# Optimization experiments

Measured on AMD Instinct MI355X. Metric: run time of the kernel, lower is better.

## Reference

```python
import jax, jax.numpy as jnp
import numpy as np

DT = 1.0          # ODENet default dt
W_SCALE = 0.05    # keep forward-Euler trajectory numerically tame


def setup_inputs() -> dict:
    key = jax.random.key(0)
    ks = jax.random.split(key, 4)
    T, B, H = 8192, 128, 128
    x = jax.random.normal(ks[0], (T, B, 1), dtype=jnp.float32)
    W1 = jax.random.normal(ks[1], (2, H), dtype=jnp.float32) * W_SCALE
    b1 = jnp.zeros((H,), dtype=jnp.float32)
    W2 = jax.random.normal(ks[2], (H, H), dtype=jnp.float32) * W_SCALE
    b2 = jnp.zeros((H,), dtype=jnp.float32)
    W3 = jax.random.normal(ks[3], (H, 1), dtype=jnp.float32) * W_SCALE
    b3 = jnp.zeros((1,), dtype=jnp.float32)
    return {"x": x, "W1": W1, "b1": b1, "W2": W2, "b2": b2, "W3": W3, "b3": b3}


def reference(x, W1, b1, W2, b2, W3, b3):
    # x: (T, B, 1). State y: (B,), init zeros (initial_value in ODENet.forward).
    # Forward Euler: y_{n+1} = y_n + dt * f(x_n, y_n), returning all T states
    # (y_0 included), i.e. output shape (T, B, 1) matching the input shape.
    x_sq = x[..., 0]                      # (T, B) == self.derivative_network.input
    B = x_sq.shape[1]
    y0 = jnp.zeros((B,), dtype=x.dtype)   # initial_value

    def deriv(xt, y):
        inp = jnp.stack([xt, y], axis=-1)          # (B, 2)
        h = jnp.tanh(inp @ W1 + b1)                # (B, H)
        h = jnp.tanh(h @ W2 + b2)                  # (B, H)
        return (h @ W3 + b3)[..., 0]               # (B,)

    def step(y, xt):
        y_next = y + DT * deriv(xt, y)
        return y_next, y_next

    # T-1 Euler steps produce states y_1..y_{T-1}
    _, ys = jax.lax.scan(step, y0, x_sq[:-1])      # (T-1, B)
    out = jnp.concatenate([y0[None], ys], axis=0)  # (T, B)
    return out[..., None]                          # (T, B, 1)
```

## Files before the change

### kernel.cpp

```cpp
#include <hip/hip_runtime.h>

#define T_STEPS 8192
#define BATCH   128
#define HID     128
#define NTHR    512

typedef float v2f __attribute__((ext_vector_type(2)));

__device__ __forceinline__ float fast_tanh(float z) {
    float e = __expf(2.0f * z);
    float r = __builtin_amdgcn_rcpf(1.0f + e);
    return fmaf(-2.0f, r, 1.0f);
}

__device__ __forceinline__ float quad_sum(float x) {
    int t1 = __builtin_amdgcn_update_dpp(0, __builtin_bit_cast(int, x),
                                         0xB1 , 0xf, 0xf, false);
    x += __builtin_bit_cast(float, t1);
    int t2 = __builtin_amdgcn_update_dpp(0, __builtin_bit_cast(int, x),
                                         0x4E , 0xf, 0xf, false);
    x += __builtin_bit_cast(float, t2);
    return x;
}

__device__ __forceinline__ float wave_sum_quaduniform(float x) {
#define DPP_ADD(ctrl) do {                                                        \
        int t_ = __builtin_amdgcn_update_dpp(0, __builtin_bit_cast(int, x),       \
                                             (ctrl), 0xf, 0xf, false);            \
        x += __builtin_bit_cast(float, t_); } while (0)
    DPP_ADD(0x114);
    DPP_ADD(0x118);
    DPP_ADD(0x142);
    DPP_ADD(0x143);
#undef DPP_ADD
    int s_ = __builtin_amdgcn_readlane(__builtin_bit_cast(int, x), 63);
    return __builtin_bit_cast(float, s_);
}

__device__ __forceinline__ float bcast_lane(float v, int l) {
    int r = __builtin_amdgcn_readlane(__builtin_bit_cast(int, v), l);
    return __builtin_bit_cast(float, r);
}

#define FORALL16(M) M(0) M(1) M(2) M(3) M(4) M(5) M(6) M(7) \
                    M(8) M(9) M(10) M(11) M(12) M(13) M(14) M(15)

__global__ __launch_bounds__(NTHR, 2) void odenet_scan(
    const float* __restrict__ x,
    const float* __restrict__ W1, const float* __restrict__ b1,
    const float* __restrict__ W2, const float* __restrict__ b2,
    const float* __restrict__ W3, const float* __restrict__ b3,
    float* __restrict__ out) {

    const int b    = blockIdx.x;
    const int tid  = threadIdx.x;
    const int w    = tid >> 6;
    const int lane = tid & 63;
    const int j    = (w << 4) | (lane >> 2);
    const int s    = lane & 3;

    __shared__ __align__(16) float h1buf[8][144];
    __shared__ __align__(16) float dyx[2][8];

    const float* col = W2 + j;
    const int kb = s << 5;
#define DECLW(i) v2f wp##i = {col[(kb + 2*(i) + 0) * HID],                        \
                              col[(kb + 2*(i) + 1) * HID]};
    FORALL16(DECLW)
#undef DECLW
#define PINW(i) asm volatile("" : "+v"(wp##i));
    FORALL16(PINW)
#undef PINW

    float w1xa = W1[lane],      w1ya = W1[HID + lane],      b1a = b1[lane];
    float w1xb = W1[lane + 64], w1yb = W1[HID + lane + 64], b1b = b1[lane + 64];
    float b2j = b2[j], w3j = W3[j], b3v = b3[0];
    asm volatile("" : "+v"(w1xa), "+v"(w1ya), "+v"(b1a),
                      "+v"(w1xb), "+v"(w1yb), "+v"(b1b),
                      "+v"(b2j), "+v"(w3j), "+v"(b3v));

    float y    = 0.0f;
    float ybuf = 0.0f;
    if (w == 0 && lane == 0) out[b] = 0.0f;

    float xbuf  = x[lane * BATCH + b];
    int   nb    = 64;
    float xnext = x[min(nb + lane, T_STEPS - 1) * BATCH + b];
    float xv = bcast_lane(xbuf, 0);
    float ax = fmaf(xv, w1xa, b1a);
    float bx = fmaf(xv, w1xb, b1b);

    const float4* h4 = (const float4*)&h1buf[w][s * 36];

    for (int t = 0; t < T_STEPS - 1; ++t) {
        const int tm = t & 63;

        float ha = fast_tanh(fmaf(y, w1ya, ax));
        float hb = fast_tanh(fmaf(y, w1yb, bx));
        h1buf[w][((lane >> 5)    ) * 36 + (lane & 31)] = ha;
        h1buf[w][((lane >> 5) + 2) * 36 + (lane & 31)] = hb;

        v2f a0 = {0.f, 0.f}, a1 = {0.f, 0.f}, a2 = {0.f, 0.f}, a3 = {0.f, 0.f};
        {
            float4 q0 = h4[0], q1 = h4[1], q2 = h4[2], q3 = h4[3];
            float4 q4 = h4[4], q5 = h4[5], q6 = h4[6], q7 = h4[7];
            v2f h0 = {q0.x, q0.y}, h1_ = {q0.z, q0.w};
            v2f h2 = {q1.x, q1.y}, h3 = {q1.z, q1.w};
            v2f h4v = {q2.x, q2.y}, h5 = {q2.z, q2.w};
            v2f h6 = {q3.x, q3.y}, h7 = {q3.z, q3.w};
            v2f h8 = {q4.x, q4.y}, h9 = {q4.z, q4.w};
            v2f hA = {q5.x, q5.y}, hB = {q5.z, q5.w};
            v2f hC = {q6.x, q6.y}, hD = {q6.z, q6.w};
            v2f hE = {q7.x, q7.y}, hF = {q7.z, q7.w};
            a0 += wp0 * h0;  a1 += wp1 * h1_; a2 += wp2 * h2;  a3 += wp3 * h3;
            a0 += wp4 * h4v; a1 += wp5 * h5;  a2 += wp6 * h6;  a3 += wp7 * h7;
            a0 += wp8 * h8;  a1 += wp9 * h9;  a2 += wp10 * hA; a3 += wp11 * hB;
            a0 += wp12 * hC; a1 += wp13 * hD; a2 += wp14 * hE; a3 += wp15 * hF;
        }
        v2f ap = (a0 + a1) + (a2 + a3);

        float z2  = quad_sum(ap.x + ap.y);
        float h2  = fast_tanh(z2 + b2j);
        float dyw = wave_sum_quaduniform(w3j * h2);

        if (lane == 0) dyx[t & 1][w] = dyw;

        const int tmn = (t + 1) & 63;
        if (tmn == 0) {
            xbuf = xnext;
            nb += 64;
            xnext = x[min(nb + lane, T_STEPS - 1) * BATCH + b];
        }
        float xvn = bcast_lane(xbuf, tmn);
        float axn = fmaf(xvn, w1xa, b1a);
        float bxn = fmaf(xvn, w1xb, b1b);

        asm volatile("s_waitcnt lgkmcnt(0)\n\ts_barrier" ::: "memory");

        const float4* dx4 = (const float4*)dyx[t & 1];
        float4 r0 = dx4[0], r1 = dx4[1];
        y += ((r0.x + r0.y) + (r0.z + r0.w))
           + ((r1.x + r1.y) + (r1.z + r1.w)) + b3v;

        ybuf = (lane == tm) ? y : ybuf;
        if (w == 0 && tm == 63)
            out[(t - 62 + lane) * BATCH + b] = ybuf;

        ax = axn; bx = bxn;
    }
    if (w == 0 && lane < 63)
        out[(T_STEPS - 63 + lane) * BATCH + b] = ybuf;
}

extern "C" void kernel_launch(void* const* d_in, const int* in_sizes, int n_in,
                              void* d_out, int out_size, void* d_ws, size_t ws_size,
                              hipStream_t stream) {
    const float* x  = (const float*)d_in[0];
    const float* W1 = (const float*)d_in[1];
    const float* b1 = (const float*)d_in[2];
    const float* W2 = (const float*)d_in[3];
    const float* b2 = (const float*)d_in[4];
    const float* W3 = (const float*)d_in[5];
    const float* b3 = (const float*)d_in[6];

    odenet_scan<<<dim3(BATCH), dim3(NTHR), 0, stream>>>(
        x, W1, b1, W2, b2, W3, b3, (float*)d_out);
}
```

Before: 4.015 ms.

## Halve block to 4 waves with 2-way K split per hidden unit

Each block now uses 256 threads (4 waves) instead of 512. Each lane holds 64 W2 weights in registers, and two lanes share one hidden unit where four did before. The cross-lane reduction shrinks from a quad sum to a pair sum, and the final wave reduction writes from lane 63 with no readlane. The per-step barrier synchronises fewer waves and sums fewer partials. In exchange, each lane's serial FMA chain doubles in length and register pressure rises.

After: 4.010 ms. About the same (-0.1%).

```diff
diff --git a/kernel.cpp b/kernel.cpp
--- a/kernel.cpp
+++ b/kernel.cpp
@@ -3,7 +3,7 @@
 #define T_STEPS 8192
 #define BATCH   128
 #define HID     128
-#define NTHR    512
+#define NTHR    256
 
 typedef float v2f __attribute__((ext_vector_type(2)));
 
@@ -13,28 +13,25 @@
     return fmaf(-2.0f, r, 1.0f);
 }
 
-__device__ __forceinline__ float quad_sum(float x) {
+__device__ __forceinline__ float pair_sum(float x) {
     int t1 = __builtin_amdgcn_update_dpp(0, __builtin_bit_cast(int, x),
-                                         0xB1 , 0xf, 0xf, false);
-    x += __builtin_bit_cast(float, t1);
-    int t2 = __builtin_amdgcn_update_dpp(0, __builtin_bit_cast(int, x),
-                                         0x4E , 0xf, 0xf, false);
-    x += __builtin_bit_cast(float, t2);
-    return x;
+                                         0xB1 ,
+                                         0xf, 0xf, false);
+    return x + __builtin_bit_cast(float, t1);
 }
 
-__device__ __forceinline__ float wave_sum_quaduniform(float x) {
+__device__ __forceinline__ float wave_sum_pairuniform_l63(float x) {
 #define DPP_ADD(ctrl) do {                                                        \
         int t_ = __builtin_amdgcn_update_dpp(0, __builtin_bit_cast(int, x),       \
                                              (ctrl), 0xf, 0xf, false);            \
         x += __builtin_bit_cast(float, t_); } while (0)
+    DPP_ADD(0x112);
     DPP_ADD(0x114);
     DPP_ADD(0x118);
     DPP_ADD(0x142);
     DPP_ADD(0x143);
 #undef DPP_ADD
-    int s_ = __builtin_amdgcn_readlane(__builtin_bit_cast(int, x), 63);
-    return __builtin_bit_cast(float, s_);
+    return x;
 }
 
 __device__ __forceinline__ float bcast_lane(float v, int l) {
@@ -42,8 +39,10 @@
     return __builtin_bit_cast(float, r);
 }
 
-#define FORALL16(M) M(0) M(1) M(2) M(3) M(4) M(5) M(6) M(7) \
-                    M(8) M(9) M(10) M(11) M(12) M(13) M(14) M(15)
+#define FORALL32(M) M(0) M(1) M(2) M(3) M(4) M(5) M(6) M(7) \
+                    M(8) M(9) M(10) M(11) M(12) M(13) M(14) M(15) \
+                    M(16) M(17) M(18) M(19) M(20) M(21) M(22) M(23) \
+                    M(24) M(25) M(26) M(27) M(28) M(29) M(30) M(31)
 
 __global__ __launch_bounds__(NTHR, 2) void odenet_scan(
     const float* __restrict__ x,
@@ -56,20 +55,20 @@
     const int tid  = threadIdx.x;
     const int w    = tid >> 6;
     const int lane = tid & 63;
-    const int j    = (w << 4) | (lane >> 2);
-    const int s    = lane & 3;
+    const int j    = (w << 5) | (lane >> 1);
+    const int s    = lane & 1;
 
-    __shared__ __align__(16) float h1buf[8][144];
-    __shared__ __align__(16) float dyx[2][8];
+    __shared__ __align__(16) float h1buf[4][136];
+    __shared__ __align__(16) float dyx[2][4];
 
     const float* col = W2 + j;
-    const int kb = s << 5;
+    const int kb = s << 6;
 #define DECLW(i) v2f wp##i = {col[(kb + 2*(i) + 0) * HID],                        \
                               col[(kb + 2*(i) + 1) * HID]};
-    FORALL16(DECLW)
+    FORALL32(DECLW)
 #undef DECLW
 #define PINW(i) asm volatile("" : "+v"(wp##i));
-    FORALL16(PINW)
+    FORALL32(PINW)
 #undef PINW
 
     float w1xa = W1[lane],      w1ya = W1[HID + lane],      b1a = b1[lane];
@@ -90,40 +89,38 @@
     float ax = fmaf(xv, w1xa, b1a);
     float bx = fmaf(xv, w1xb, b1b);
 
-    const float4* h4 = (const float4*)&h1buf[w][s * 36];
+    const float4* h4 = (const float4*)&h1buf[w][s * 68];
 
     for (int t = 0; t < T_STEPS - 1; ++t) {
         const int tm = t & 63;
 
         float ha = fast_tanh(fmaf(y, w1ya, ax));
         float hb = fast_tanh(fmaf(y, w1yb, bx));
-        h1buf[w][((lane >> 5)    ) * 36 + (lane & 31)] = ha;
-        h1buf[w][((lane >> 5) + 2) * 36 + (lane & 31)] = hb;
+        h1buf[w][lane]      = ha;
+        h1buf[w][68 + lane] = hb;
 
         v2f a0 = {0.f, 0.f}, a1 = {0.f, 0.f}, a2 = {0.f, 0.f}, a3 = {0.f, 0.f};
         {
-            float4 q0 = h4[0], q1 = h4[1], q2 = h4[2], q3 = h4[3];
-            float4 q4 = h4[4], q5 = h4[5], q6 = h4[6], q7 = h4[7];
-            v2f h0 = {q0.x, q0.y}, h1_ = {q0.z, q0.w};
-            v2f h2 = {q1.x, q1.y}, h3 = {q1.z, q1.w};
-            v2f h4v = {q2.x, q2.y}, h5 = {q2.z, q2.w};
-            v2f h6 = {q3.x, q3.y}, h7 = {q3.z, q3.w};
-            v2f h8 = {q4.x, q4.y}, h9 = {q4.z, q4.w};
-            v2f hA = {q5.x, q5.y}, hB = {q5.z, q5.w};
-            v2f hC = {q6.x, q6.y}, hD = {q6.z, q6.w};
-            v2f hE = {q7.x, q7.y}, hF = {q7.z, q7.w};
-            a0 += wp0 * h0;  a1 += wp1 * h1_; a2 += wp2 * h2;  a3 += wp3 * h3;
-            a0 += wp4 * h4v; a1 += wp5 * h5;  a2 += wp6 * h6;  a3 += wp7 * h7;
-            a0 += wp8 * h8;  a1 += wp9 * h9;  a2 += wp10 * hA; a3 += wp11 * hB;
-            a0 += wp12 * hC; a1 += wp13 * hD; a2 += wp14 * hE; a3 += wp15 * hF;
+            float4 q;
+#define FMAP(qi, WA, WB, AA, AB) q = h4[qi];                                      \
+            { v2f lo = {q.x, q.y}, hi = {q.z, q.w};                               \
+              AA += WA * lo; AB += WB * hi; }
+            FMAP( 0, wp0 , wp1 , a0, a1) FMAP( 1, wp2 , wp3 , a2, a3)
+            FMAP( 2, wp4 , wp5 , a0, a1) FMAP( 3, wp6 , wp7 , a2, a3)
+            FMAP( 4, wp8 , wp9 , a0, a1) FMAP( 5, wp10, wp11, a2, a3)
+            FMAP( 6, wp12, wp13, a0, a1) FMAP( 7, wp14, wp15, a2, a3)
+            FMAP( 8, wp16, wp17, a0, a1) FMAP( 9, wp18, wp19, a2, a3)
+            FMAP(10, wp20, wp21, a0, a1) FMAP(11, wp22, wp23, a2, a3)
+            FMAP(12, wp24, wp25, a0, a1) FMAP(13, wp26, wp27, a2, a3)
+            FMAP(14, wp28, wp29, a0, a1) FMAP(15, wp30, wp31, a2, a3)
+#undef FMAP
         }
         v2f ap = (a0 + a1) + (a2 + a3);
 
-        float z2  = quad_sum(ap.x + ap.y);
+        float z2  = pair_sum(ap.x + ap.y);
         float h2  = fast_tanh(z2 + b2j);
-        float dyw = wave_sum_quaduniform(w3j * h2);
-
-        if (lane == 0) dyx[t & 1][w] = dyw;
+        float dyw = wave_sum_pairuniform_l63(w3j * h2);
+        if (lane == 63) dyx[t & 1][w] = dyw;
 
         const int tmn = (t + 1) & 63;
         if (tmn == 0) {
@@ -137,10 +134,8 @@
 
         asm volatile("s_waitcnt lgkmcnt(0)\n\ts_barrier" ::: "memory");
 
-        const float4* dx4 = (const float4*)dyx[t & 1];
-        float4 r0 = dx4[0], r1 = dx4[1];
-        y += ((r0.x + r0.y) + (r0.z + r0.w))
-           + ((r1.x + r1.y) + (r1.z + r1.w)) + b3v;
+        float4 d = *(const float4*)&dyx[t & 1][0];
+        y += ((d.x + d.y) + (d.z + d.w)) + b3v;
 
         ybuf = (lane == tm) ? y : ybuf;
         if (w == 0 && tm == 63)
```
